# Optimization experiments

Hardware: AMD Instinct MI355X
Metric: run time of the kernel (lower is better)

Reference implementation:

```python
import jax, jax.numpy as jnp
import numpy as np

N, E = 50000, 800000
IN_DIM, OUT_DIM, NHEAD = 256, 64, 4
SLOPE = 0.2
BN_EPS = 1e-5


def setup_inputs() -> dict:
    key = jax.random.key(0)
    ks = jax.random.split(key, 12)
    HD = NHEAD * OUT_DIM
    s = 1.0 / np.sqrt(IN_DIM)
    inp = {
        'feat': jax.random.normal(ks[0], (N, IN_DIM), dtype=jnp.float32),
        'src': jax.random.randint(ks[1], (E,), 0, N, dtype=jnp.int32),
        'dst': jax.random.randint(ks[2], (E,), 0, N, dtype=jnp.int32),
        # GATv2Conv params (DGL: separate src/dst linear, per-head attn vector, output bias)
        'W_src': jax.random.normal(ks[3], (IN_DIM, HD), dtype=jnp.float32) * s,
        'b_src': jnp.zeros((HD,), dtype=jnp.float32),
        'W_dst': jax.random.normal(ks[4], (IN_DIM, HD), dtype=jnp.float32) * s,
        'b_dst': jnp.zeros((HD,), dtype=jnp.float32),
        'attn': jax.random.normal(ks[5], (NHEAD, OUT_DIM), dtype=jnp.float32) * (1.0 / np.sqrt(OUT_DIM)),
        'out_bias': jnp.zeros((HD,), dtype=jnp.float32),
        # trailing fc: Linear(HD -> OUT_DIM) + BatchNorm1d + LeakyReLU (dropout = identity in eval)
        'fc_W': jax.random.normal(ks[6], (HD, OUT_DIM), dtype=jnp.float32) * (1.0 / np.sqrt(HD)),
        'fc_b': jnp.zeros((OUT_DIM,), dtype=jnp.float32),
        'gamma': jnp.ones((OUT_DIM,), dtype=jnp.float32),
        'beta': jnp.zeros((OUT_DIM,), dtype=jnp.float32),
    }
    return inp


def _leaky(x):
    return jnp.where(x >= 0, x, SLOPE * x)


def reference(feat, src, dst, W_src, b_src, W_dst, b_dst, attn, out_bias, fc_W, fc_b, gamma, beta):
    H, D = NHEAD, OUT_DIM
    h_src = (feat @ W_src + b_src).reshape(N, H, D)
    h_dst = (feat @ W_dst + b_dst).reshape(N, H, D)
    # per-edge GATv2 score: attn . LeakyReLU(h_src[u] + h_dst[v])
    hs_e = h_src[src]                                   # [E,H,D]
    e = jnp.einsum('ehd,hd->eh', _leaky(hs_e + h_dst[dst]), attn)  # [E,H]
    # segment softmax over incoming edges of each dst node
    m = jax.ops.segment_max(e, dst, num_segments=N)     # [N,H]
    ex = jnp.exp(e - m[dst])
    denom = jax.ops.segment_sum(ex, dst, num_segments=N)
    a = ex / denom[dst]                                 # [E,H]
    # weighted scatter-add aggregation
    rst = jax.ops.segment_sum(a[:, :, None] * hs_e, dst, num_segments=N)  # [N,H,D]
    rst = rst + out_bias.reshape(H, D)
    # trailing fc + BatchNorm1d (batch stats) + LeakyReLU
    z = rst.reshape(N, H * D) @ fc_W + fc_b
    mu = jnp.mean(z, axis=0)
    var = jnp.var(z, axis=0)
    z = (z - mu) * jax.lax.rsqrt(var + BN_EPS) * gamma + beta
    return _leaky(z)
```

## Files before the change

### kernel.cpp

```cpp
#include <hip/hip_runtime.h>
#include <math.h>

#define N_NODES 50000
#define N_EDGES 800000
#define HD 256
#define OUT_DIM 64
#define NHEAD 4
#define SLOPE 0.2f
#define BN_EPS 1e-5f
#define LOG2E 1.4426950408889634f
#define NTILES 391

typedef __attribute__((ext_vector_type(8))) short short8;
typedef __attribute__((ext_vector_type(4))) float float4v;

__device__ __forceinline__ float leaky(float x) { return x >= 0.f ? x : SLOPE * x; }

__device__ __forceinline__ float bf2f(unsigned short u) {
    return __uint_as_float(((unsigned)u) << 16);
}
__device__ __forceinline__ unsigned short f2bf(float f) {
    unsigned u = __float_as_uint(f);
    unsigned r = (u + 0x7fffu + ((u >> 16) & 1u)) >> 16;
    return (unsigned short)r;
}

template <int CTRL>
__device__ __forceinline__ float ror_add(float v) {
    const int r = __builtin_amdgcn_update_dpp(0, __float_as_int(v), CTRL, 0xF, 0xF, true);
    return v + __int_as_float(r);
}
__device__ __forceinline__ float group16_sum(float v) {
    v = ror_add<0x121>(v);
    v = ror_add<0x122>(v);
    v = ror_add<0x124>(v);
    v = ror_add<0x128>(v);
    return v;
}

__global__ __launch_bounds__(256) void prep_kernel(const float* __restrict__ feat,
                                                   const float* __restrict__ W_src,
                                                   const float* __restrict__ W_dst,
                                                   const float* __restrict__ fc_W,
                                                   unsigned short* __restrict__ feat_bf,
                                                   unsigned short* __restrict__ WtS,
                                                   unsigned short* __restrict__ WtD,
                                                   unsigned short* __restrict__ WtF,
                                                   int* __restrict__ cnt2,
                                                   float* __restrict__ sums,
                                                   int* __restrict__ done) {
    const int b = blockIdx.x;
    const int t = threadIdx.x;
    if (b < 12500) {
        const int i = b * 256 + t;
        const float4 v = ((const float4*)feat)[i];
        ushort4 o;
        o.x = f2bf(v.x); o.y = f2bf(v.y); o.z = f2bf(v.z); o.w = f2bf(v.w);
        ((ushort4*)feat_bf)[i] = o;
    } else if (b < 12756) {
        const int n = b - 12500;
        WtS[(size_t)n * 256 + t] = f2bf(W_src[(size_t)t * 256 + n]);
    } else if (b < 13012) {
        const int n = b - 12756;
        WtD[(size_t)n * 256 + t] = f2bf(W_dst[(size_t)t * 256 + n]);
    } else if (b < 13076) {
        const int n = b - 13012;
        WtF[(size_t)n * 256 + t] = f2bf(fc_W[(size_t)t * 64 + n]);
    } else if (b < 13174) {
        const int i = (b - 13076) * 256 + t;
        if (i < 25000) ((int4*)cnt2)[i] = make_int4(0, 0, 0, 0);
    } else {
        if (t < 128) sums[t] = 0.f;
        if (t == 128) done[0] = 0;
    }
}

__global__ __launch_bounds__(256) void proj_kernel(const unsigned short* __restrict__ A,
                                                   const unsigned short* __restrict__ BtS,
                                                   const unsigned short* __restrict__ BtD,
                                                   const float* __restrict__ bS,
                                                   const float* __restrict__ bD,
                                                   unsigned short* __restrict__ CS,
                                                   unsigned short* __restrict__ CD) {
    __shared__ unsigned short Bs[64 * 256];

    const int t    = threadIdx.x;
    const int w    = t >> 6;
    const int lane = t & 63;
    const int q    = lane >> 4;
    const int l16  = lane & 15;
    const int c0   = (blockIdx.y & 3) * 64;
    const bool isD = (blockIdx.y >= 4);

    const unsigned short* Bt   = isD ? BtD : BtS;
    const float*          bias = isD ? bD  : bS;
    unsigned short*       C    = isD ? CD  : CS;

    {
        const int r   = t >> 2;
        const int seg = t & 3;
        const int c   = r >> 4;
        const int L   = r & 15;
        const unsigned short* g = Bt + (size_t)(c0 + r) * 256 + seg * 64;
#pragma unroll
        for (int kk2 = 0; kk2 < 2; ++kk2) {
            const int kk = seg * 2 + kk2;
#pragma unroll
            for (int q2 = 0; q2 < 4; ++q2)
                *(short8*)(&Bs[((c * 8 + kk) * 64 + q2 * 16 + L) * 8]) =
                    *(const short8*)(g + kk2 * 32 + q2 * 8);
        }
    }
    __syncthreads();

    float vb[4];
#pragma unroll
    for (int c = 0; c < 4; ++c) vb[c] = bias[c0 + c * 16 + l16];

    for (int tile = blockIdx.x; tile < NTILES; tile += 98) {
        const int m0 = tile * 128;

        int ar0 = m0 + w * 32 + l16;
        int ar1 = ar0 + 16;
        if (ar0 > N_NODES - 1) ar0 = N_NODES - 1;
        if (ar1 > N_NODES - 1) ar1 = N_NODES - 1;
        const unsigned short* Ab0 = A + (size_t)ar0 * 256 + q * 8;
        const unsigned short* Ab1 = A + (size_t)ar1 * 256 + q * 8;
        short8 afr0[8], afr1[8];
#pragma unroll
        for (int kk = 0; kk < 8; ++kk) {
            afr0[kk] = *(const short8*)(Ab0 + kk * 32);
            afr1[kk] = *(const short8*)(Ab1 + kk * 32);
        }

        float4v a0[4] = {}, a1[4] = {};
#pragma unroll
        for (int kk = 0; kk < 8; ++kk) {
            const short8 af0 = afr0[kk];
            const short8 af1 = afr1[kk];
#pragma unroll
            for (int c = 0; c < 4; ++c) {
                const short8 b = *(const short8*)(&Bs[((c * 8 + kk) * 64 + lane) * 8]);
                a0[c] = __builtin_amdgcn_mfma_f32_16x16x32_bf16(af0, b, a0[c], 0, 0, 0);
                a1[c] = __builtin_amdgcn_mfma_f32_16x16x32_bf16(af1, b, a1[c], 0, 0, 0);
            }
        }

#pragma unroll
        for (int c = 0; c < 4; ++c) {
            const int col = c0 + c * 16 + l16;
#pragma unroll
            for (int i = 0; i < 4; ++i) {
                const int r0 = m0 + w * 32 + q * 4 + i;
                const int r1 = r0 + 16;
                if (r0 < N_NODES) C[(size_t)r0 * 256 + col] = f2bf(a0[c][i] + vb[c]);
                if (r1 < N_NODES) C[(size_t)r1 * 256 + col] = f2bf(a1[c][i] + vb[c]);
            }
        }
    }
}

__global__ __launch_bounds__(256) void fc_bn_kernel(const unsigned short* __restrict__ A,
                                                    const unsigned short* __restrict__ Bt,
                                                    const float* __restrict__ bias,
                                                    float* __restrict__ C,
                                                    float* __restrict__ sums,
                                                    int M) {
    const int w    = threadIdx.x >> 6;
    const int lane = threadIdx.x & 63;
    const int q    = lane >> 4;
    const int l16  = lane & 15;
    const int m0   = blockIdx.x * 64;
    const int t    = threadIdx.x;

    __shared__ float ssum[64], ssq[64];
    if (t < 64) { ssum[t] = 0.f; ssq[t] = 0.f; }

    int arow = m0 + w * 16 + l16;
    if (arow > M - 1) arow = M - 1;
    const unsigned short* Ab  = A  + (size_t)arow * 256 + q * 8;
    const unsigned short* Btb = Bt + (size_t)l16 * 256 + q * 8;

    float4v acc[4] = {};

    for (int k0 = 0; k0 < 256; k0 += 32) {
        const short8 af = *(const short8*)(Ab + k0);
#pragma unroll
        for (int c = 0; c < 4; ++c) {
            const short8 bf = *(const short8*)(Btb + (size_t)c * 16 * 256 + k0);
            acc[c] = __builtin_amdgcn_mfma_f32_16x16x32_bf16(af, bf, acc[c], 0, 0, 0);
        }
    }
    __syncthreads();

#pragma unroll
    for (int c = 0; c < 4; ++c) {
        const int col = c * 16 + l16;
        const float b = bias[col];
        float s = 0.f, qq = 0.f;
#pragma unroll
        for (int i = 0; i < 4; ++i) {
            const int r = m0 + w * 16 + q * 4 + i;
            if (r < M) {
                const float v = acc[c][i] + b;
                C[(size_t)r * 64 + col] = v;
                s += v;
                qq += v * v;
            }
        }
        atomicAdd(&ssum[col], s);
        atomicAdd(&ssq[col], qq);
    }
    __syncthreads();
    if (t < 64) {
        atomicAdd(&sums[t], ssum[t]);
        atomicAdd(&sums[64 + t], ssq[t]);
    }
}

__global__ void hist_kernel(const int* __restrict__ dst, int* __restrict__ cnt) {
    const int i = blockIdx.x * 256 + threadIdx.x;
    if (i < N_EDGES) atomicAdd(&cnt[dst[i]], 1);
}

__global__ __launch_bounds__(512) void scan_kernel(const int* __restrict__ cnt,
                                                   int* __restrict__ offs,
                                                   int* __restrict__ bsum,
                                                   int* __restrict__ bpre,
                                                   int* __restrict__ done) {
    __shared__ int s[512];
    __shared__ bool amLast;
    const int t = threadIdx.x;
    const int i = blockIdx.x * 512 + t;
    const int v = (i < N_NODES) ? cnt[i] : 0;
    s[t] = v;
    __syncthreads();
    for (int off = 1; off < 512; off <<= 1) {
        const int x = (t >= off) ? s[t - off] : 0;
        __syncthreads();
        s[t] += x;
        __syncthreads();
    }
    if (i < N_NODES) offs[i] = s[t] - v;
    if (t == 511) {
        bsum[blockIdx.x] = s[511];
        __threadfence();
        amLast = (atomicAdd(done, 1) == (int)gridDim.x - 1);
    }
    __syncthreads();
    if (amLast) {
        const int v2 = (t < (int)gridDim.x) ? atomicAdd(&bsum[t], 0) : 0;
        s[t] = v2;
        __syncthreads();
        for (int off = 1; off < 512; off <<= 1) {
            const int x = (t >= off) ? s[t - off] : 0;
            __syncthreads();
            s[t] += x;
            __syncthreads();
        }
        if (t < (int)gridDim.x) bpre[t] = s[t] - v2;
    }
}

__global__ void scatter_kernel(const int* __restrict__ src,
                               const int* __restrict__ dst,
                               const int* __restrict__ offs,
                               const int* __restrict__ bpre,
                               int* __restrict__ cursor,
                               int* __restrict__ srcl) {
    const int i = blockIdx.x * 256 + threadIdx.x;
    if (i < N_EDGES) {
        const int d = dst[i];
        const int p = offs[d] + bpre[d >> 9] + atomicAdd(&cursor[d], 1);
        srcl[p] = src[i];
    }
}

__global__ __launch_bounds__(256) void agg_fused_kernel(const unsigned short* __restrict__ h_src,
                                                        const unsigned short* __restrict__ h_dst,
                                                        const int* __restrict__ srcl,
                                                        const int* __restrict__ offs,
                                                        const int* __restrict__ bpre,
                                                        const float* __restrict__ attn,
                                                        const float* __restrict__ out_bias,
                                                        unsigned short* __restrict__ rst) {
    const int node = blockIdx.x * 4 + (threadIdx.x >> 6);
    const int lane = threadIdx.x & 63;
    const int d4 = lane * 4;

    const int beg = offs[node] + bpre[node >> 9];
    const int end = (node + 1 == N_NODES) ? N_EDGES
                                          : (offs[node + 1] + bpre[(node + 1) >> 9]);

    const ushort4 hdv = *(const ushort4*)(h_dst + (size_t)node * 256 + d4);
    const float hd0 = bf2f(hdv.x), hd1 = bf2f(hdv.y), hd2 = bf2f(hdv.z), hd3 = bf2f(hdv.w);
    const float4 araw = *(const float4*)(attn + d4);
    const float av0 = araw.x * LOG2E, av1 = araw.y * LOG2E,
                av2 = araw.z * LOG2E, av3 = araw.w * LOG2E;
    const float aw0 = av0 * SLOPE, aw1 = av1 * SLOPE,
                aw2 = av2 * SLOPE, aw3 = av3 * SLOPE;

    float wsum = 0.f, a0 = 0.f, a1 = 0.f, a2 = 0.f, a3 = 0.f;

#define EDGE_BODY(sreg)                                                          \
    {                                                                            \
        const unsigned short* row = h_src + (size_t)(sreg) * 256;                \
        const ushort4 va = *(const ushort4*)(row + d4);                          \
        const float r0 = bf2f(va.x), r1 = bf2f(va.y);                            \
        const float r2 = bf2f(va.z), r3 = bf2f(va.w);                            \
        const float y0 = r0 + hd0, y1 = r1 + hd1, y2 = r2 + hd2, y3 = r3 + hd3;  \
        float pp = av0 * fmaxf(y0, 0.f) + aw0 * fminf(y0, 0.f);                  \
        pp = fmaf(av1, fmaxf(y1, 0.f), fmaf(aw1, fminf(y1, 0.f), pp));           \
        pp = fmaf(av2, fmaxf(y2, 0.f), fmaf(aw2, fminf(y2, 0.f), pp));           \
        pp = fmaf(av3, fmaxf(y3, 0.f), fmaf(aw3, fminf(y3, 0.f), pp));           \
        pp = group16_sum(pp);                                                    \
        const float wg = __builtin_amdgcn_exp2f(pp);                             \
        wsum += wg;                                                              \
        a0 = fmaf(wg, r0, a0);                                                   \
        a1 = fmaf(wg, r1, a1);                                                   \
        a2 = fmaf(wg, r2, a2);                                                   \
        a3 = fmaf(wg, r3, a3);                                                   \
    }

    int p = beg;
    const int nfull = (end - beg) >> 2;
    for (int it = 0; it < nfull; ++it, p += 4) {
        const int s0 = __builtin_amdgcn_readfirstlane(srcl[p]);
        const int s1 = __builtin_amdgcn_readfirstlane(srcl[p + 1]);
        const int s2 = __builtin_amdgcn_readfirstlane(srcl[p + 2]);
        const int s3 = __builtin_amdgcn_readfirstlane(srcl[p + 3]);
        EDGE_BODY(s0);
        EDGE_BODY(s1);
        EDGE_BODY(s2);
        EDGE_BODY(s3);
    }
    for (; p < end; ++p) {
        const int s0 = __builtin_amdgcn_readfirstlane(srcl[p]);
        EDGE_BODY(s0);
    }
#undef EDGE_BODY

    const float inv = (wsum > 0.f) ? 1.f / wsum : 0.f;
    const float4 ob = *(const float4*)(out_bias + d4);
    ushort4 o;
    o.x = f2bf(fmaf(a0, inv, ob.x));
    o.y = f2bf(fmaf(a1, inv, ob.y));
    o.z = f2bf(fmaf(a2, inv, ob.z));
    o.w = f2bf(fmaf(a3, inv, ob.w));
    *(ushort4*)(rst + (size_t)node * 256 + d4) = o;
}

__global__ void bn_final_kernel(float* __restrict__ z,
                                const float* __restrict__ sums,
                                const float* __restrict__ gamma,
                                const float* __restrict__ beta) {
    const int i = blockIdx.x * 256 + threadIdx.x;
    if (i < N_NODES * 64) {
        const int col = i & 63;
        const float mu  = sums[col] * (1.f / N_NODES);
        const float var = sums[64 + col] * (1.f / N_NODES) - mu * mu;
        const float v = (z[i] - mu) * rsqrtf(var + BN_EPS) * gamma[col] + beta[col];
        z[i] = leaky(v);
    }
}

extern "C" void kernel_launch(void* const* d_in, const int* in_sizes, int n_in,
                              void* d_out, int out_size, void* d_ws, size_t ws_size,
                              hipStream_t stream) {
    const float* feat    = (const float*)d_in[0];
    const int*   src     = (const int*)  d_in[1];
    const int*   dst     = (const int*)  d_in[2];
    const float* W_src   = (const float*)d_in[3];
    const float* b_src   = (const float*)d_in[4];
    const float* W_dst   = (const float*)d_in[5];
    const float* b_dst   = (const float*)d_in[6];
    const float* attn    = (const float*)d_in[7];
    const float* out_bias= (const float*)d_in[8];
    const float* fc_W    = (const float*)d_in[9];
    const float* fc_b    = (const float*)d_in[10];
    const float* gamma   = (const float*)d_in[11];
    const float* beta    = (const float*)d_in[12];
    float* z = (float*)d_out;

    char* ws = (char*)d_ws;
    size_t off = 0;
    auto carve = [&](size_t bytes) -> void* {
        void* p = ws + off;
        off = (off + bytes + 255) & ~(size_t)255;
        return p;
    };
    unsigned short* feat_bf = (unsigned short*)carve((size_t)N_NODES * 256 * 2);
    unsigned short* h_src_bf= (unsigned short*)carve((size_t)N_NODES * 256 * 2);
    unsigned short* h_dst_bf= (unsigned short*)carve((size_t)N_NODES * 256 * 2);
    unsigned short* rst_bf  = (unsigned short*)carve((size_t)N_NODES * 256 * 2);
    unsigned short* WtS     = (unsigned short*)carve((size_t)256 * 256 * 2);
    unsigned short* WtD     = (unsigned short*)carve((size_t)256 * 256 * 2);
    unsigned short* WtF     = (unsigned short*)carve((size_t)64 * 256 * 2);
    int*   srcl   = (int*)  carve((size_t)N_EDGES * 4);
    int*   cnt    = (int*)  carve((size_t)2 * N_NODES * 4);
    int*   cursor = cnt + N_NODES;
    int*   offs   = (int*)  carve((size_t)(N_NODES + 1) * 4);
    int*   bsum   = (int*)  carve(128 * 4);
    int*   bpre   = (int*)  carve(128 * 4);
    float* sums   = (float*)carve(128 * 4);
    int*   done   = (int*)  carve(64);

    const int nchunks = (N_NODES + 511) / 512;

    prep_kernel<<<13175, 256, 0, stream>>>(feat, W_src, W_dst, fc_W,
                                           feat_bf, WtS, WtD, WtF, cnt, sums, done);

    proj_kernel<<<dim3(98, 8), 256, 0, stream>>>(
        feat_bf, WtS, WtD, b_src, b_dst, h_src_bf, h_dst_bf);

    hist_kernel<<<(N_EDGES + 255) / 256, 256, 0, stream>>>(dst, cnt);
    scan_kernel<<<nchunks, 512, 0, stream>>>(cnt, offs, bsum, bpre, done);
    scatter_kernel<<<(N_EDGES + 255) / 256, 256, 0, stream>>>(src, dst, offs, bpre, cursor, srcl);

    agg_fused_kernel<<<N_NODES / 4, 256, 0, stream>>>(h_src_bf, h_dst_bf, srcl, offs, bpre,
                                                      attn, out_bias, rst_bf);

    fc_bn_kernel<<<(N_NODES + 63) / 64, 256, 0, stream>>>(rst_bf, WtF, fc_b, z, sums, N_NODES);

    bn_final_kernel<<<(N_NODES * 64 + 255) / 256, 256, 0, stream>>>(z, sums, gamma, beta);
}
```

Baseline: 358.1 us.

## Fuse histogram into projection, fold BN finalize into fc via grid barrier, cheapen leaky

```diff
diff --git a/kernel.cpp b/kernel.cpp
--- a/kernel.cpp
+++ b/kernel.cpp
@@ -72,6 +72,7 @@
     } else {
         if (t < 128) sums[t] = 0.f;
         if (t == 128) done[0] = 0;
+        if (t == 129) done[1] = 0;
     }
 }
 
@@ -81,16 +82,25 @@
                                                    const float* __restrict__ bS,
                                                    const float* __restrict__ bD,
                                                    unsigned short* __restrict__ CS,
-                                                   unsigned short* __restrict__ CD) {
+                                                   unsigned short* __restrict__ CD,
+                                                   const int* __restrict__ dst,
+                                                   int* __restrict__ cnt) {
     __shared__ unsigned short Bs[64 * 256];
+
+    if (blockIdx.y == 0) {
+        for (int i = blockIdx.x * 256 + threadIdx.x; i < N_EDGES; i += 98 * 256)
+            atomicAdd(&cnt[dst[i]], 1);
+        return;
+    }
 
     const int t    = threadIdx.x;
     const int w    = t >> 6;
     const int lane = t & 63;
     const int q    = lane >> 4;
     const int l16  = lane & 15;
-    const int c0   = (blockIdx.y & 3) * 64;
-    const bool isD = (blockIdx.y >= 4);
+    const int yy   = blockIdx.y - 1;
+    const int c0   = (yy & 3) * 64;
+    const bool isD = (yy >= 4);
 
     const unsigned short* Bt   = isD ? BtD : BtS;
     const float*          bias = isD ? bD  : bS;
@@ -160,12 +170,15 @@
     }
 }
 
-__global__ __launch_bounds__(256) void fc_bn_kernel(const unsigned short* __restrict__ A,
-                                                    const unsigned short* __restrict__ Bt,
-                                                    const float* __restrict__ bias,
-                                                    float* __restrict__ C,
-                                                    float* __restrict__ sums,
-                                                    int M) {
+__global__ __launch_bounds__(256, 4) void fc_bn_kernel(const unsigned short* __restrict__ A,
+                                                       const unsigned short* __restrict__ Bt,
+                                                       const float* __restrict__ bias,
+                                                       float* __restrict__ C,
+                                                       float* __restrict__ sums,
+                                                       const float* __restrict__ gamma,
+                                                       const float* __restrict__ beta,
+                                                       int* __restrict__ done2,
+                                                       int M) {
     const int w    = threadIdx.x >> 6;
     const int lane = threadIdx.x & 63;
     const int q    = lane >> 4;
@@ -193,6 +206,7 @@
     }
     __syncthreads();
 
+    float vreg[16];
 #pragma unroll
     for (int c = 0; c < 4; ++c) {
         const int col = c * 16 + l16;
@@ -201,12 +215,9 @@
 #pragma unroll
         for (int i = 0; i < 4; ++i) {
             const int r = m0 + w * 16 + q * 4 + i;
-            if (r < M) {
-                const float v = acc[c][i] + b;
-                C[(size_t)r * 64 + col] = v;
-                s += v;
-                qq += v * v;
-            }
+            const float v = acc[c][i] + b;
+            vreg[c * 4 + i] = v;
+            if (r < M) { s += v; qq += v * v; }
         }
         atomicAdd(&ssum[col], s);
         atomicAdd(&ssq[col], qq);
@@ -216,11 +227,30 @@
         atomicAdd(&sums[t], ssum[t]);
         atomicAdd(&sums[64 + t], ssq[t]);
     }
-}
-
-__global__ void hist_kernel(const int* __restrict__ dst, int* __restrict__ cnt) {
-    const int i = blockIdx.x * 256 + threadIdx.x;
-    if (i < N_EDGES) atomicAdd(&cnt[dst[i]], 1);
+    __threadfence();
+    __syncthreads();
+    if (t == 0) {
+        __hip_atomic_fetch_add(done2, 1, __ATOMIC_ACQ_REL, __HIP_MEMORY_SCOPE_AGENT);
+        while (__hip_atomic_load(done2, __ATOMIC_ACQUIRE, __HIP_MEMORY_SCOPE_AGENT) < (int)gridDim.x)
+            __builtin_amdgcn_s_sleep(2);
+    }
+    __syncthreads();
+
+#pragma unroll
+    for (int c = 0; c < 4; ++c) {
+        const int col = c * 16 + l16;
+        const float s  = __hip_atomic_load(&sums[col], __ATOMIC_RELAXED, __HIP_MEMORY_SCOPE_AGENT);
+        const float sq = __hip_atomic_load(&sums[64 + col], __ATOMIC_RELAXED, __HIP_MEMORY_SCOPE_AGENT);
+        const float mu  = s * (1.f / N_NODES);
+        const float var = sq * (1.f / N_NODES) - mu * mu;
+        const float sc  = rsqrtf(var + BN_EPS) * gamma[col];
+        const float sh  = beta[col] - mu * sc;
+#pragma unroll
+        for (int i = 0; i < 4; ++i) {
+            const int r = m0 + w * 16 + q * 4 + i;
+            if (r < M) C[(size_t)r * 64 + col] = leaky(fmaf(vreg[c * 4 + i], sc, sh));
+        }
+    }
 }
 
 __global__ __launch_bounds__(512) void scan_kernel(const int* __restrict__ cnt,
@@ -292,27 +322,33 @@
     const int end = (node + 1 == N_NODES) ? N_EDGES
                                           : (offs[node + 1] + bpre[(node + 1) >> 9]);
 
-    const ushort4 hdv = *(const ushort4*)(h_dst + (size_t)node * 256 + d4);
-    const float hd0 = bf2f(hdv.x), hd1 = bf2f(hdv.y), hd2 = bf2f(hdv.z), hd3 = bf2f(hdv.w);
+    const uint2 hdu = *(const uint2*)(h_dst + (size_t)node * 256 + d4);
+    const float hd0 = __uint_as_float(hdu.x << 16);
+    const float hd1 = __uint_as_float(hdu.x & 0xffff0000u);
+    const float hd2 = __uint_as_float(hdu.y << 16);
+    const float hd3 = __uint_as_float(hdu.y & 0xffff0000u);
+
     const float4 araw = *(const float4*)(attn + d4);
-    const float av0 = araw.x * LOG2E, av1 = araw.y * LOG2E,
-                av2 = araw.z * LOG2E, av3 = araw.w * LOG2E;
-    const float aw0 = av0 * SLOPE, aw1 = av1 * SLOPE,
-                aw2 = av2 * SLOPE, aw3 = av3 * SLOPE;
+    const float c10 = araw.x * (0.6f * LOG2E), c20 = araw.x * (0.4f * LOG2E);
+    const float c11 = araw.y * (0.6f * LOG2E), c21 = araw.y * (0.4f * LOG2E);
+    const float c12 = araw.z * (0.6f * LOG2E), c22 = araw.z * (0.4f * LOG2E);
+    const float c13 = araw.w * (0.6f * LOG2E), c23 = araw.w * (0.4f * LOG2E);
 
     float wsum = 0.f, a0 = 0.f, a1 = 0.f, a2 = 0.f, a3 = 0.f;
 
 #define EDGE_BODY(sreg)                                                          \
     {                                                                            \
         const unsigned short* row = h_src + (size_t)(sreg) * 256;                \
-        const ushort4 va = *(const ushort4*)(row + d4);                          \
-        const float r0 = bf2f(va.x), r1 = bf2f(va.y);                            \
-        const float r2 = bf2f(va.z), r3 = bf2f(va.w);                            \
+        const uint2 u = *(const uint2*)(row + d4);                               \
+        const float r0 = __uint_as_float(u.x << 16);                             \
+        const float r1 = __uint_as_float(u.x & 0xffff0000u);                     \
+        const float r2 = __uint_as_float(u.y << 16);                             \
+        const float r3 = __uint_as_float(u.y & 0xffff0000u);                     \
         const float y0 = r0 + hd0, y1 = r1 + hd1, y2 = r2 + hd2, y3 = r3 + hd3;  \
-        float pp = av0 * fmaxf(y0, 0.f) + aw0 * fminf(y0, 0.f);                  \
-        pp = fmaf(av1, fmaxf(y1, 0.f), fmaf(aw1, fminf(y1, 0.f), pp));           \
-        pp = fmaf(av2, fmaxf(y2, 0.f), fmaf(aw2, fminf(y2, 0.f), pp));           \
-        pp = fmaf(av3, fmaxf(y3, 0.f), fmaf(aw3, fminf(y3, 0.f), pp));           \
+        float pp = fmaf(c10, y0, c20 * __builtin_fabsf(y0));                     \
+        pp = fmaf(c11, y1, fmaf(c21, __builtin_fabsf(y1), pp));                  \
+        pp = fmaf(c12, y2, fmaf(c22, __builtin_fabsf(y2), pp));                  \
+        pp = fmaf(c13, y3, fmaf(c23, __builtin_fabsf(y3), pp));                  \
         pp = group16_sum(pp);                                                    \
         const float wg = __builtin_amdgcn_exp2f(pp);                             \
         wsum += wg;                                                              \
@@ -348,20 +384,6 @@
     o.z = f2bf(fmaf(a2, inv, ob.z));
     o.w = f2bf(fmaf(a3, inv, ob.w));
     *(ushort4*)(rst + (size_t)node * 256 + d4) = o;
-}
-
-__global__ void bn_final_kernel(float* __restrict__ z,
-                                const float* __restrict__ sums,
-                                const float* __restrict__ gamma,
-                                const float* __restrict__ beta) {
-    const int i = blockIdx.x * 256 + threadIdx.x;
-    if (i < N_NODES * 64) {
-        const int col = i & 63;
-        const float mu  = sums[col] * (1.f / N_NODES);
-        const float var = sums[64 + col] * (1.f / N_NODES) - mu * mu;
-        const float v = (z[i] - mu) * rsqrtf(var + BN_EPS) * gamma[col] + beta[col];
-        z[i] = leaky(v);
-    }
 }
 
 extern "C" void kernel_launch(void* const* d_in, const int* in_sizes, int n_in,
@@ -410,17 +432,15 @@
     prep_kernel<<<13175, 256, 0, stream>>>(feat, W_src, W_dst, fc_W,
                                            feat_bf, WtS, WtD, WtF, cnt, sums, done);
 
-    proj_kernel<<<dim3(98, 8), 256, 0, stream>>>(
-        feat_bf, WtS, WtD, b_src, b_dst, h_src_bf, h_dst_bf);
-
-    hist_kernel<<<(N_EDGES + 255) / 256, 256, 0, stream>>>(dst, cnt);
+    proj_kernel<<<dim3(98, 9), 256, 0, stream>>>(
+        feat_bf, WtS, WtD, b_src, b_dst, h_src_bf, h_dst_bf, dst, cnt);
+
     scan_kernel<<<nchunks, 512, 0, stream>>>(cnt, offs, bsum, bpre, done);
     scatter_kernel<<<(N_EDGES + 255) / 256, 256, 0, stream>>>(src, dst, offs, bpre, cursor, srcl);
 
     agg_fused_kernel<<<N_NODES / 4, 256, 0, stream>>>(h_src_bf, h_dst_bf, srcl, offs, bpre,
                                                       attn, out_bias, rst_bf);
 
-    fc_bn_kernel<<<(N_NODES + 63) / 64, 256, 0, stream>>>(rst_bf, WtF, fc_b, z, sums, N_NODES);
-
-    bn_final_kernel<<<(N_NODES * 64 + 255) / 256, 256, 0, stream>>>(z, sums, gamma, beta);
-}
+    fc_bn_kernel<<<(N_NODES + 63) / 64, 256, 0, stream>>>(rst_bf, WtF, fc_b, z, sums,
+                                                          gamma, beta, done + 1, N_NODES);
+}
```

Measured after the change: 414.3 us. 15.7% more time.
